# Kernel optimization log

Hardware: AMD Instinct MI355X
Metric: run time of the kernel (lower is better)

The kernel has to match this reference:

```python
import jax, jax.numpy as jnp
import numpy as np

IN_F, OUT_F, GRID = 1024, 1024, 8
B = 8192
GRID_LO, GRID_HI = -1.0, 1.0


def setup_inputs() -> dict:
    key = jax.random.key(0)
    k1, k2 = jax.random.split(key)
    x = jax.random.normal(k1, (B, IN_F), dtype=jnp.float32)
    # buffers: grid is linspace expanded over in_features; sigma = 1.5*h
    h = (GRID_HI - GRID_LO) / (GRID - 1)
    grid = jnp.broadcast_to(jnp.linspace(GRID_LO, GRID_HI, GRID, dtype=jnp.float32), (IN_F, GRID))
    sigma = jnp.float32(1.5 * h)
    # params
    scale_base = jnp.ones((IN_F, OUT_F), dtype=jnp.float32)
    scale_spline = jnp.ones((IN_F, OUT_F), dtype=jnp.float32)
    # kaiming_uniform-ish init: bound = sqrt(6/fan_in)/sqrt(1+a^2) approximated by small uniform
    fan_in = IN_F * GRID
    gain = np.sqrt(2.0 / (1.0 + 5.0 * 0.1 * 0.1))
    bound = gain * np.sqrt(3.0 / fan_in)
    spline_weight = jax.random.uniform(k2, (OUT_F, IN_F, GRID), dtype=jnp.float32, minval=-bound, maxval=bound)
    return {"x": x, "scale_base": scale_base, "spline_weight": spline_weight,
            "scale_spline": scale_spline, "grid": grid, "sigma": sigma}


def reference(x, scale_base, spline_weight, scale_spline, grid, sigma):
    # x: [B, I]; grid: [I, G]; spline_weight: [O, I, G]; scales: [I, O]
    base_out = jnp.einsum('bi,io->bo', jax.nn.silu(x), scale_base)
    # RBF bases: exp(-((x - grid)/sigma)^2)  -> [B, I, G]
    bases = jnp.exp(-jnp.square((x[:, :, None] - grid[None, :, :]) / sigma))
    # fused spline contraction (mathematically identical to big,oig->bio then bio,io->bo)
    spline_out = jnp.einsum('big,oig,io->bo', bases, spline_weight, scale_spline)
    return base_out + spline_out
```

## Files before the change

kernel.cpp:

```cpp
#include <hip/hip_runtime.h>


#define BATCH 8192
#define IN_F  1024
#define OUT_F 1024
#define GRID_N 8
#define K2    (IN_F * GRID_N)
#define KTOT  (IN_F + K2)

#define BM 128
#define BN 128
#define BK 64
#define BK8 128

typedef __bf16 bf16x8 __attribute__((ext_vector_type(8)));
typedef float  f32x4  __attribute__((ext_vector_type(4)));
typedef int    int32x8 __attribute__((ext_vector_type(8)));

__device__ __forceinline__ void gl2lds16(const void* g, void* l) {
  __builtin_amdgcn_global_load_lds(
      (const __attribute__((address_space(1))) void*)g,
      (__attribute__((address_space(3))) void*)l, 16, 0, 0);
}

__device__ __forceinline__ void pack_fp8x8(const float* v, int& w0, int& w1) {
  w0 = 0; w1 = 0;
  w0 = __builtin_amdgcn_cvt_pk_fp8_f32(v[0], v[1], w0, false);
  w0 = __builtin_amdgcn_cvt_pk_fp8_f32(v[2], v[3], w0, true);
  w1 = __builtin_amdgcn_cvt_pk_fp8_f32(v[4], v[5], w1, false);
  w1 = __builtin_amdgcn_cvt_pk_fp8_f32(v[6], v[7], w1, true);
}

__global__ __launch_bounds__(256)
void kan_mix(const float* __restrict__ x, const float* __restrict__ sb,
             const float* __restrict__ sw, const float* __restrict__ ss,
             const float* __restrict__ grid, const float* __restrict__ sigma,
             __bf16* __restrict__ sbT, unsigned char* __restrict__ wbt8,
             unsigned char* __restrict__ Ab8, __bf16* __restrict__ sbA) {
  const int t = threadIdx.x;
  const int bx = blockIdx.x;
  if (bx < 256) {
    __shared__ float tile[64][65];
    const int o0 = (bx & 15) * 64, k0 = (bx >> 4) * 64;
    const int r = t >> 4, c4 = (t & 15) * 4;
    #pragma unroll
    for (int it = 0; it < 4; ++it) {
      const int k = k0 + r + it * 16;
      float4 v = *(const float4*)(sb + (size_t)k * OUT_F + o0 + c4);
      tile[r + it * 16][c4 + 0] = v.x; tile[r + it * 16][c4 + 1] = v.y;
      tile[r + it * 16][c4 + 2] = v.z; tile[r + it * 16][c4 + 3] = v.w;
    }
    __syncthreads();
    #pragma unroll
    for (int it = 0; it < 4; ++it) {
      const int ol = r + it * 16;
      union { __bf16 h[4]; uint2 q; } s;
      #pragma unroll
      for (int e = 0; e < 4; ++e) s.h[e] = (__bf16)tile[c4 + e][ol];
      *(uint2*)(sbT + (size_t)(o0 + ol) * IN_F + k0 + c4) = s.q;
    }
  } else if (bx < 512) {
    __shared__ float tile[64][65];
    const int sp = bx - 256;
    const int o0 = (sp >> 4) * 64;
    const int j0 = (sp & 15) * 512;
    const int i0 = j0 >> 3;
    const int r = t >> 4, c4 = (t & 15) * 4;
    #pragma unroll
    for (int it = 0; it < 4; ++it) {
      const int i = i0 + r + it * 16;
      float4 v = *(const float4*)(ss + (size_t)i * OUT_F + o0 + c4);
      tile[r + it * 16][c4 + 0] = v.x; tile[r + it * 16][c4 + 1] = v.y;
      tile[r + it * 16][c4 + 2] = v.z; tile[r + it * 16][c4 + 3] = v.w;
    }
    __syncthreads();
    #pragma unroll
    for (int p = 0; p < 16; ++p) {
      const int f = p * 256 + t;
      const int o_l = f >> 6, i_l = f & 63;
      const float sc = tile[i_l][o_l];
      const float* swp = sw + (size_t)(o0 + o_l) * K2 + j0 + i_l * 8;
      float4 a = *(const float4*)swp;
      float4 b = *(const float4*)(swp + 4);
      float vv[8] = {a.x * sc, a.y * sc, a.z * sc, a.w * sc,
                     b.x * sc, b.y * sc, b.z * sc, b.w * sc};
      int w0, w1; pack_fp8x8(vv, w0, w1);
      *(int2*)(wbt8 + (size_t)(o0 + o_l) * K2 + j0 + i_l * 8) = make_int2(w0, w1);
    }
  } else {
    const int b = bx - 512;
    const float inv_sigma = 1.0f / sigma[0];
    const float* xrow = x + (size_t)b * IN_F;
    unsigned char* arow = Ab8 + (size_t)b * K2;
    __bf16* srow = sbA + (size_t)b * IN_F;
    {
      float4 v = ((const float4*)xrow)[t];
      float vv[4] = {v.x, v.y, v.z, v.w};
      union { __bf16 h[4]; uint2 q; } s;
      #pragma unroll
      for (int e = 0; e < 4; ++e) s.h[e] = (__bf16)(vv[e] / (1.0f + __expf(-vv[e])));
      ((uint2*)srow)[t] = s.q;
    }
    #pragma unroll
    for (int it = 0; it < 4; ++it) {
      const int i = t + it * 256;
      const float u = xrow[i];
      float4 g0 = *(const float4*)(grid + (size_t)i * GRID_N);
      float4 g1 = *(const float4*)(grid + (size_t)i * GRID_N + 4);
      float gg[8] = {g0.x, g0.y, g0.z, g0.w, g1.x, g1.y, g1.z, g1.w};
      float bb[8];
      #pragma unroll
      for (int g = 0; g < GRID_N; ++g) {
        float d = (u - gg[g]) * inv_sigma;
        bb[g] = __expf(-d * d);
      }
      int w0, w1; pack_fp8x8(bb, w0, w1);
      *(int2*)(arow + (size_t)i * GRID_N) = make_int2(w0, w1);
    }
  }
}

__global__ __launch_bounds__(256)
void kan_gemm_all(const unsigned char* __restrict__ Ab8,
                  const unsigned char* __restrict__ wbt8,
                  const __bf16* __restrict__ sbA,
                  const __bf16* __restrict__ sbT,
                  float* __restrict__ out) {
  __shared__ unsigned char As8[BM * BK8];
  __shared__ unsigned char Bs8[BN * BK8];
  __bf16* As16 = (__bf16*)As8;
  __bf16* Bs16 = (__bf16*)Bs8;

  const int tid = threadIdx.x;
  const int bx  = blockIdx.x;
  const int s   = bx >> 3;
  const int r0  = ((bx & 7) * 8 + (s >> 3)) * BM;
  const int c0  = (s & 7) * BN;

  const int lane = tid & 63, wave = tid >> 6;
  const int wm = wave & 1, wn = wave >> 1;
  const int quad = lane >> 4, l15 = lane & 15;

  int a_off8[4][2], b_off8[4][2];
  #pragma unroll
  for (int t4 = 0; t4 < 4; ++t4) {
    const int rowA = wm * 64 + t4 * 16 + l15;
    const int rowB = wn * 64 + t4 * 16 + l15;
    #pragma unroll
    for (int h = 0; h < 2; ++h) {
      a_off8[t4][h] = rowA * BK8 + (((quad * 2 + h) ^ (rowA & 7)) * 16);
      b_off8[t4][h] = rowB * BK8 + (((quad * 2 + h) ^ (rowB & 7)) * 16);
    }
  }
  int a_off16[2][4], b_off16[2][4];
  #pragma unroll
  for (int ks = 0; ks < 2; ++ks) {
    const int kc = ks * 4 + quad;
    #pragma unroll
    for (int t4 = 0; t4 < 4; ++t4) {
      const int rowA = wm * 64 + t4 * 16 + l15;
      a_off16[ks][t4] = (rowA * 8 + (kc ^ (rowA & 7))) * 8;
      const int rowB = wn * 64 + t4 * 16 + l15;
      b_off16[ks][t4] = (rowB * 8 + (kc ^ (rowB & 7))) * 8;
    }
  }
  const unsigned char* aSrc8[4]; const unsigned char* bSrc8[4];
  const __bf16* aSrc16[4]; const __bf16* bSrc16[4]; int dstOff[4];
  #pragma unroll
  for (int it = 0; it < 4; ++it) {
    const int p = it * 256 + tid;
    const int row = p >> 3;
    const int kc  = (p & 7) ^ (row & 7);
    aSrc8[it]  = Ab8  + (size_t)(r0 + row) * K2 + kc * 16;
    bSrc8[it]  = wbt8 + (size_t)(c0 + row) * K2 + kc * 16;
    aSrc16[it] = sbA  + (size_t)(r0 + row) * IN_F + kc * 8;
    bSrc16[it] = sbT  + (size_t)(c0 + row) * IN_F + kc * 8;
    dstOff[it] = p * 16;
  }

  f32x4 zero; zero[0] = 0.f; zero[1] = 0.f; zero[2] = 0.f; zero[3] = 0.f;
  f32x4 acc[4][4];
  #pragma unroll
  for (int a = 0; a < 4; ++a)
    #pragma unroll
    for (int b = 0; b < 4; ++b) acc[a][b] = zero;

  for (int kb = 0; kb < K2; kb += BK8) {
    __syncthreads();
    #pragma unroll
    for (int it = 0; it < 4; ++it) {
      gl2lds16(aSrc8[it] + kb, &As8[dstOff[it]]);
      gl2lds16(bSrc8[it] + kb, &Bs8[dstOff[it]]);
    }
    __syncthreads();
    union frag { int32x8 v; uint4 q[2]; };
    frag af[4], bfv[4];
    #pragma unroll
    for (int t4 = 0; t4 < 4; ++t4) {
      af[t4].q[0]  = *(const uint4*)&As8[a_off8[t4][0]];
      af[t4].q[1]  = *(const uint4*)&As8[a_off8[t4][1]];
      bfv[t4].q[0] = *(const uint4*)&Bs8[b_off8[t4][0]];
      bfv[t4].q[1] = *(const uint4*)&Bs8[b_off8[t4][1]];
    }
    #pragma unroll
    for (int tm = 0; tm < 4; ++tm)
      #pragma unroll
      for (int tn = 0; tn < 4; ++tn)
        acc[tm][tn] = __builtin_amdgcn_mfma_scale_f32_16x16x128_f8f6f4(
            af[tm].v, bfv[tn].v, acc[tm][tn],
            0, 0, 0, 0x7F7F7F7F, 0, 0x7F7F7F7F);
  }

  for (int kb = 0; kb < IN_F; kb += BK) {
    __syncthreads();
    #pragma unroll
    for (int it = 0; it < 4; ++it) {
      gl2lds16(aSrc16[it] + kb, (char*)As16 + dstOff[it]);
      gl2lds16(bSrc16[it] + kb, (char*)Bs16 + dstOff[it]);
    }
    __syncthreads();
    #pragma unroll
    for (int ks = 0; ks < 2; ++ks) {
      bf16x8 af[4], bfv[4];
      #pragma unroll
      for (int t4 = 0; t4 < 4; ++t4) af[t4]  = *(const bf16x8*)&As16[a_off16[ks][t4]];
      #pragma unroll
      for (int t4 = 0; t4 < 4; ++t4) bfv[t4] = *(const bf16x8*)&Bs16[b_off16[ks][t4]];
      #pragma unroll
      for (int tm = 0; tm < 4; ++tm)
        #pragma unroll
        for (int tn = 0; tn < 4; ++tn)
          acc[tm][tn] = __builtin_amdgcn_mfma_f32_16x16x32_bf16(
              af[tm], bfv[tn], acc[tm][tn], 0, 0, 0);
    }
  }

  #pragma unroll
  for (int tm = 0; tm < 4; ++tm) {
    const int row = r0 + wm * 64 + tm * 16 + quad * 4;
    #pragma unroll
    for (int tn = 0; tn < 4; ++tn) {
      const int col = c0 + wn * 64 + tn * 16 + l15;
      float* op = out + (size_t)row * OUT_F + col;
      #pragma unroll
      for (int r = 0; r < 4; ++r)
        op[(size_t)r * OUT_F] = acc[tm][tn][r];
    }
  }
}

__global__ __launch_bounds__(256)
void kan_prep_w_full(const float* __restrict__ sb, const float* __restrict__ sw,
                     const float* __restrict__ ss, __bf16* __restrict__ wbt) {
  const int t = threadIdx.x;
  if (blockIdx.x < 256) {
    __shared__ float tile[64][65];
    const int o0 = (blockIdx.x & 15) * 64, k0 = (blockIdx.x >> 4) * 64;
    const int r = t >> 4, c4 = (t & 15) * 4;
    #pragma unroll
    for (int it = 0; it < 4; ++it) {
      const int k = k0 + r + it * 16;
      float4 v = *(const float4*)(sb + (size_t)k * OUT_F + o0 + c4);
      tile[r + it * 16][c4 + 0] = v.x; tile[r + it * 16][c4 + 1] = v.y;
      tile[r + it * 16][c4 + 2] = v.z; tile[r + it * 16][c4 + 3] = v.w;
    }
    __syncthreads();
    #pragma unroll
    for (int it = 0; it < 4; ++it) {
      const int ol = r + it * 16;
      union { __bf16 h[4]; uint2 q; } s;
      #pragma unroll
      for (int e = 0; e < 4; ++e) s.h[e] = (__bf16)tile[c4 + e][ol];
      *(uint2*)(wbt + (size_t)(o0 + ol) * KTOT + k0 + c4) = s.q;
    }
  } else {
    const size_t e = ((size_t)(blockIdx.x - 256) * 256 + t) * 8;
    const int o = (int)(e >> 13);
    const int j = (int)(e & 8191);
    const int i = j >> 3;
    const float sc = ss[(size_t)i * OUT_F + o];
    float4 a = *(const float4*)(sw + e);
    float4 b = *(const float4*)(sw + e + 4);
    float vv[8] = {a.x, a.y, a.z, a.w, b.x, b.y, b.z, b.w};
    union { __bf16 h[8]; uint4 q; } s;
    #pragma unroll
    for (int g = 0; g < 8; ++g) s.h[g] = (__bf16)(vv[g] * sc);
    *(uint4*)(wbt + (size_t)o * KTOT + IN_F + j) = s.q;
  }
}

__global__ __launch_bounds__(256, 2)
void kan_gemm_fused(const float* __restrict__ x, const __bf16* __restrict__ wbt,
                    const float* __restrict__ grid, const float* __restrict__ sigma,
                    float* __restrict__ out) {
  __shared__ __bf16 As[BM * BK];
  __shared__ __bf16 Bs[BN * BK];
  __shared__ float  gLds[IN_F * GRID_N];
  const int tid = threadIdx.x;
  const int bx  = blockIdx.x;
  const int c0  = (bx & 7) * BN;
  const int r0  = (bx >> 3) * BM;
  for (int idx = tid; idx < IN_F * GRID_N / 4; idx += 256)
    ((float4*)gLds)[idx] = ((const float4*)grid)[idx];
  const float inv_sigma = 1.0f / sigma[0];
  const int lane = tid & 63, wave = tid >> 6;
  const int wm = wave & 1, wn = wave >> 1;
  const int quad = lane >> 4, l15 = lane & 15;
  f32x4 zero; zero[0] = 0.f; zero[1] = 0.f; zero[2] = 0.f; zero[3] = 0.f;
  f32x4 acc[4][4];
  #pragma unroll
  for (int a = 0; a < 4; ++a)
    #pragma unroll
    for (int b = 0; b < 4; ++b) acc[a][b] = zero;
  const int m = tid >> 1, half = tid & 1;
  const float* xrow = x + (size_t)(r0 + m) * IN_F;
  __syncthreads();
  for (int kb = 0; kb < KTOT; kb += BK) {
    union { __bf16 h[32]; uint4 q[4]; } av;
    if (kb < IN_F) {
      const float4* xp = (const float4*)(xrow + kb + half * 32);
      #pragma unroll
      for (int j4 = 0; j4 < 8; ++j4) {
        float4 v = xp[j4];
        float vv[4] = {v.x, v.y, v.z, v.w};
        #pragma unroll
        for (int e = 0; e < 4; ++e)
          av.h[j4 * 4 + e] = (__bf16)(vv[e] / (1.0f + __expf(-vv[e])));
      }
    } else {
      const int i0 = (kb - IN_F) >> 3;
      float4 xv = *(const float4*)(xrow + i0 + half * 4);
      float xs[4] = {xv.x, xv.y, xv.z, xv.w};
      #pragma unroll
      for (int ii = 0; ii < 4; ++ii) {
        const float u = xs[ii];
        const float* gp = &gLds[(i0 + half * 4 + ii) * GRID_N];
        #pragma unroll
        for (int g = 0; g < GRID_N; ++g) {
          float d = (u - gp[g]) * inv_sigma;
          av.h[ii * 8 + g] = (__bf16)__expf(-d * d);
        }
      }
    }
    __syncthreads();
    {
      uint4* dst = (uint4*)&As[m * BK + half * 32];
      #pragma unroll
      for (int qd = 0; qd < 4; ++qd) dst[qd] = av.q[qd];
    }
    #pragma unroll
    for (int it = 0; it < 4; ++it) {
      const int idx = it * 2048 + tid * 8;
      const int n = idx >> 6, k = idx & 63;
      gl2lds16(wbt + (size_t)(c0 + n) * KTOT + kb + k, &Bs[idx]);
    }
    __syncthreads();
    #pragma unroll
    for (int ks = 0; ks < 2; ++ks) {
      bf16x8 af[4], bfv[4];
      #pragma unroll
      for (int t4 = 0; t4 < 4; ++t4)
        af[t4] = *(const bf16x8*)&As[(wm * 64 + t4 * 16 + l15) * BK + ks * 32 + quad * 8];
      #pragma unroll
      for (int t4 = 0; t4 < 4; ++t4)
        bfv[t4] = *(const bf16x8*)&Bs[(wn * 64 + t4 * 16 + l15) * BK + ks * 32 + quad * 8];
      #pragma unroll
      for (int tm = 0; tm < 4; ++tm)
        #pragma unroll
        for (int tn = 0; tn < 4; ++tn)
          acc[tm][tn] = __builtin_amdgcn_mfma_f32_16x16x32_bf16(
              af[tm], bfv[tn], acc[tm][tn], 0, 0, 0);
    }
  }
  #pragma unroll
  for (int tm = 0; tm < 4; ++tm) {
    const int row = r0 + wm * 64 + tm * 16 + quad * 4;
    #pragma unroll
    for (int tn = 0; tn < 4; ++tn) {
      const int col = c0 + wn * 64 + tn * 16 + l15;
      float* op = out + (size_t)row * OUT_F + col;
      #pragma unroll
      for (int r = 0; r < 4; ++r)
        op[(size_t)r * OUT_F] = acc[tm][tn][r];
    }
  }
}

extern "C" void kernel_launch(void* const* d_in, const int* in_sizes, int n_in,
                              void* d_out, int out_size, void* d_ws, size_t ws_size,
                              hipStream_t stream) {
  const float* x     = (const float*)d_in[0];
  const float* sb    = (const float*)d_in[1];
  const float* sw    = (const float*)d_in[2];
  const float* ss    = (const float*)d_in[3];
  const float* grid  = (const float*)d_in[4];
  const float* sigma = (const float*)d_in[5];
  float* out = (float*)d_out;

  const size_t SBT_BYTES = (size_t)OUT_F * IN_F * 2;
  const size_t WS_BYTES  = (size_t)OUT_F * K2;
  const size_t A_BYTES   = (size_t)BATCH * K2;
  const size_t SBA_BYTES = (size_t)BATCH * IN_F * 2;

  if (ws_size >= SBT_BYTES + WS_BYTES + A_BYTES + SBA_BYTES) {
    __bf16*        sbT  = (__bf16*)d_ws;
    unsigned char* wbt8 = (unsigned char*)d_ws + SBT_BYTES;
    unsigned char* Ab8  = (unsigned char*)d_ws + SBT_BYTES + WS_BYTES;
    __bf16*        sbA  = (__bf16*)((char*)d_ws + SBT_BYTES + WS_BYTES + A_BYTES);
    kan_mix<<<dim3(512 + BATCH), dim3(256), 0, stream>>>(
        x, sb, sw, ss, grid, sigma, sbT, wbt8, Ab8, sbA);
    kan_gemm_all<<<dim3((BATCH / BM) * (OUT_F / BN)), dim3(256), 0, stream>>>(
        Ab8, wbt8, sbA, sbT, out);
  } else {
    __bf16* wbt = (__bf16*)d_ws;
    kan_prep_w_full<<<dim3(4352), dim3(256), 0, stream>>>(sb, sw, ss, wbt);
    kan_gemm_fused<<<dim3((BATCH / BM) * (OUT_F / BN)), dim3(256), 0, stream>>>(
        x, wbt, grid, sigma, out);
  }
}
```

Baseline: 221.2 us.

## Double-buffer LDS in fused KAN GEMM with 256x128 tiles and 8 waves

Restructures the combined fp8/bf16 GEMM to use two LDS buffers, so the global-to-LDS loads for the next K-slice are issued before the MFMAs on the current one, leaving one barrier per iteration instead of two. The block tile grows to 256x128 with 512 threads (4x2 waves), which halves the grid and shares each B tile across twice as many A rows. The fp8-to-bf16 phase change is handled by prefetching the first bf16 slice during the last fp8 iteration. MFMA sections are wrapped in s_setprio to favour issuing math. The cost is 96KB of LDS per block, which limits occupancy to one block per CU, and only 256 blocks in the grid.

Result: slower. 244.3 us (+10.4%).

```diff
diff --git a/kernel.cpp b/kernel.cpp
--- a/kernel.cpp
+++ b/kernel.cpp
@@ -120,25 +120,22 @@
   }
 }
 
-__global__ __launch_bounds__(256)
+__global__ __launch_bounds__(512, 2)
 void kan_gemm_all(const unsigned char* __restrict__ Ab8,
                   const unsigned char* __restrict__ wbt8,
                   const __bf16* __restrict__ sbA,
                   const __bf16* __restrict__ sbT,
                   float* __restrict__ out) {
-  __shared__ unsigned char As8[BM * BK8];
-  __shared__ unsigned char Bs8[BN * BK8];
-  __bf16* As16 = (__bf16*)As8;
-  __bf16* Bs16 = (__bf16*)Bs8;
+  __shared__ unsigned char smem[2][49152];
 
   const int tid = threadIdx.x;
   const int bx  = blockIdx.x;
-  const int s   = bx >> 3;
-  const int r0  = ((bx & 7) * 8 + (s >> 3)) * BM;
-  const int c0  = (s & 7) * BN;
+  const int xcd = bx & 7, loc = bx >> 3;
+  const int r0 = (xcd * 4 + (loc >> 3)) * 256;
+  const int c0 = (loc & 7) * 128;
 
   const int lane = tid & 63, wave = tid >> 6;
-  const int wm = wave & 1, wn = wave >> 1;
+  const int wm = wave & 3, wn = wave >> 2;
   const int quad = lane >> 4, l15 = lane & 15;
 
   int a_off8[4][2], b_off8[4][2];
@@ -148,8 +145,8 @@
     const int rowB = wn * 64 + t4 * 16 + l15;
     #pragma unroll
     for (int h = 0; h < 2; ++h) {
-      a_off8[t4][h] = rowA * BK8 + (((quad * 2 + h) ^ (rowA & 7)) * 16);
-      b_off8[t4][h] = rowB * BK8 + (((quad * 2 + h) ^ (rowB & 7)) * 16);
+      a_off8[t4][h] = rowA * 128 + (((quad * 2 + h) ^ (rowA & 7)) * 16);
+      b_off8[t4][h] = 32768 + rowB * 128 + (((quad * 2 + h) ^ (rowB & 7)) * 16);
     }
   }
   int a_off16[2][4], b_off16[2][4];
@@ -159,23 +156,31 @@
     #pragma unroll
     for (int t4 = 0; t4 < 4; ++t4) {
       const int rowA = wm * 64 + t4 * 16 + l15;
-      a_off16[ks][t4] = (rowA * 8 + (kc ^ (rowA & 7))) * 8;
+      a_off16[ks][t4] = (rowA * 8 + (kc ^ (rowA & 7))) * 16;
       const int rowB = wn * 64 + t4 * 16 + l15;
-      b_off16[ks][t4] = (rowB * 8 + (kc ^ (rowB & 7))) * 8;
-    }
-  }
-  const unsigned char* aSrc8[4]; const unsigned char* bSrc8[4];
-  const __bf16* aSrc16[4]; const __bf16* bSrc16[4]; int dstOff[4];
+      b_off16[ks][t4] = 32768 + (rowB * 8 + (kc ^ (rowB & 7))) * 16;
+    }
+  }
+
+  const unsigned char* aS8[4]; const __bf16* aS16[4]; int aD[4];
   #pragma unroll
   for (int it = 0; it < 4; ++it) {
-    const int p = it * 256 + tid;
+    const int p = it * 512 + tid;
     const int row = p >> 3;
     const int kc  = (p & 7) ^ (row & 7);
-    aSrc8[it]  = Ab8  + (size_t)(r0 + row) * K2 + kc * 16;
-    bSrc8[it]  = wbt8 + (size_t)(c0 + row) * K2 + kc * 16;
-    aSrc16[it] = sbA  + (size_t)(r0 + row) * IN_F + kc * 8;
-    bSrc16[it] = sbT  + (size_t)(c0 + row) * IN_F + kc * 8;
-    dstOff[it] = p * 16;
+    aS8[it]  = Ab8 + (size_t)(r0 + row) * K2 + kc * 16;
+    aS16[it] = sbA + (size_t)(r0 + row) * IN_F + kc * 8;
+    aD[it] = p * 16;
+  }
+  const unsigned char* bS8[2]; const __bf16* bS16[2]; int bD[2];
+  #pragma unroll
+  for (int it = 0; it < 2; ++it) {
+    const int q = it * 512 + tid;
+    const int row = q >> 3;
+    const int kc  = (q & 7) ^ (row & 7);
+    bS8[it]  = wbt8 + (size_t)(c0 + row) * K2 + kc * 16;
+    bS16[it] = sbT + (size_t)(c0 + row) * IN_F + kc * 8;
+    bD[it] = 32768 + q * 16;
   }
 
   f32x4 zero; zero[0] = 0.f; zero[1] = 0.f; zero[2] = 0.f; zero[3] = 0.f;
@@ -185,23 +190,38 @@
     #pragma unroll
     for (int b = 0; b < 4; ++b) acc[a][b] = zero;
 
-  for (int kb = 0; kb < K2; kb += BK8) {
-    __syncthreads();
-    #pragma unroll
-    for (int it = 0; it < 4; ++it) {
-      gl2lds16(aSrc8[it] + kb, &As8[dstOff[it]]);
-      gl2lds16(bSrc8[it] + kb, &Bs8[dstOff[it]]);
-    }
-    __syncthreads();
+  #pragma unroll
+  for (int it = 0; it < 4; ++it) gl2lds16(aS8[it], &smem[0][aD[it]]);
+  #pragma unroll
+  for (int it = 0; it < 2; ++it) gl2lds16(bS8[it], &smem[0][bD[it]]);
+  __syncthreads();
+
+  int cur = 0;
+  for (int t = 0; t < 64; ++t) {
+    const int nxt = cur ^ 1;
+    if (t < 63) {
+      const int kb = (t + 1) * BK8;
+      #pragma unroll
+      for (int it = 0; it < 4; ++it) gl2lds16(aS8[it] + kb, &smem[nxt][aD[it]]);
+      #pragma unroll
+      for (int it = 0; it < 2; ++it) gl2lds16(bS8[it] + kb, &smem[nxt][bD[it]]);
+    } else {
+      #pragma unroll
+      for (int it = 0; it < 4; ++it) gl2lds16(aS16[it], &smem[nxt][aD[it]]);
+      #pragma unroll
+      for (int it = 0; it < 2; ++it) gl2lds16(bS16[it], &smem[nxt][bD[it]]);
+    }
+    const unsigned char* sp = smem[cur];
     union frag { int32x8 v; uint4 q[2]; };
     frag af[4], bfv[4];
     #pragma unroll
     for (int t4 = 0; t4 < 4; ++t4) {
-      af[t4].q[0]  = *(const uint4*)&As8[a_off8[t4][0]];
-      af[t4].q[1]  = *(const uint4*)&As8[a_off8[t4][1]];
-      bfv[t4].q[0] = *(const uint4*)&Bs8[b_off8[t4][0]];
-      bfv[t4].q[1] = *(const uint4*)&Bs8[b_off8[t4][1]];
-    }
+      af[t4].q[0]  = *(const uint4*)(sp + a_off8[t4][0]);
+      af[t4].q[1]  = *(const uint4*)(sp + a_off8[t4][1]);
+      bfv[t4].q[0] = *(const uint4*)(sp + b_off8[t4][0]);
+      bfv[t4].q[1] = *(const uint4*)(sp + b_off8[t4][1]);
+    }
+    __builtin_amdgcn_s_setprio(1);
     #pragma unroll
     for (int tm = 0; tm < 4; ++tm)
       #pragma unroll
@@ -209,30 +229,39 @@
         acc[tm][tn] = __builtin_amdgcn_mfma_scale_f32_16x16x128_f8f6f4(
             af[tm].v, bfv[tn].v, acc[tm][tn],
             0, 0, 0, 0x7F7F7F7F, 0, 0x7F7F7F7F);
-  }
-
-  for (int kb = 0; kb < IN_F; kb += BK) {
-    __syncthreads();
-    #pragma unroll
-    for (int it = 0; it < 4; ++it) {
-      gl2lds16(aSrc16[it] + kb, (char*)As16 + dstOff[it]);
-      gl2lds16(bSrc16[it] + kb, (char*)Bs16 + dstOff[it]);
-    }
-    __syncthreads();
+    __builtin_amdgcn_s_setprio(0);
+    __syncthreads();
+    cur = nxt;
+  }
+
+  for (int t = 0; t < 16; ++t) {
+    const int nxt = cur ^ 1;
+    if (t < 15) {
+      const int ke = (t + 1) * BK;
+      #pragma unroll
+      for (int it = 0; it < 4; ++it) gl2lds16(aS16[it] + ke, &smem[nxt][aD[it]]);
+      #pragma unroll
+      for (int it = 0; it < 2; ++it) gl2lds16(bS16[it] + ke, &smem[nxt][bD[it]]);
+    }
+    const unsigned char* sp = smem[cur];
     #pragma unroll
     for (int ks = 0; ks < 2; ++ks) {
       bf16x8 af[4], bfv[4];
       #pragma unroll
-      for (int t4 = 0; t4 < 4; ++t4) af[t4]  = *(const bf16x8*)&As16[a_off16[ks][t4]];
-      #pragma unroll
-      for (int t4 = 0; t4 < 4; ++t4) bfv[t4] = *(const bf16x8*)&Bs16[b_off16[ks][t4]];
+      for (int t4 = 0; t4 < 4; ++t4) af[t4]  = *(const bf16x8*)(sp + a_off16[ks][t4]);
+      #pragma unroll
+      for (int t4 = 0; t4 < 4; ++t4) bfv[t4] = *(const bf16x8*)(sp + b_off16[ks][t4]);
+      __builtin_amdgcn_s_setprio(1);
       #pragma unroll
       for (int tm = 0; tm < 4; ++tm)
         #pragma unroll
         for (int tn = 0; tn < 4; ++tn)
           acc[tm][tn] = __builtin_amdgcn_mfma_f32_16x16x32_bf16(
               af[tm], bfv[tn], acc[tm][tn], 0, 0, 0);
-    }
+      __builtin_amdgcn_s_setprio(0);
+    }
+    __syncthreads();
+    cur = nxt;
   }
 
   #pragma unroll
@@ -409,7 +438,7 @@
     __bf16*        sbA  = (__bf16*)((char*)d_ws + SBT_BYTES + WS_BYTES + A_BYTES);
     kan_mix<<<dim3(512 + BATCH), dim3(256), 0, stream>>>(
         x, sb, sw, ss, grid, sigma, sbT, wbt8, Ab8, sbA);
-    kan_gemm_all<<<dim3((BATCH / BM) * (OUT_F / BN)), dim3(256), 0, stream>>>(
+    kan_gemm_all<<<dim3((BATCH / 256) * (OUT_F / 128)), dim3(512), 0, stream>>>(
         Ab8, wbt8, sbA, sbT, out);
   } else {
     __bf16* wbt = (__bf16*)d_ws;
```

## Double-buffer LDS tiles and prefetch next K-slice during MFMA compute

Applied to the files above, without the earlier changes.

Replaces the single-buffered load/sync/compute loops with a two-stage LDS ping-pong buffer. The global-to-LDS load of the next K tile is issued before the current tile is computed, and a partial vmcnt wait lets one stage of loads stay in flight. The transition from the fp8 phase to the bf16 phase is also prefetched, and MFMA sections are wrapped in s_setprio to favour compute. LDS use doubles to 64KB per block, which may reduce occupancy, and the manual waitcnt accounting is fragile.

Measured after the change: 224.8 us. Within noise of the previous version (+1.6%).

```diff
diff --git a/kernel.cpp b/kernel.cpp
--- a/kernel.cpp
+++ b/kernel.cpp
@@ -126,10 +126,7 @@
                   const __bf16* __restrict__ sbA,
                   const __bf16* __restrict__ sbT,
                   float* __restrict__ out) {
-  __shared__ unsigned char As8[BM * BK8];
-  __shared__ unsigned char Bs8[BN * BK8];
-  __bf16* As16 = (__bf16*)As8;
-  __bf16* Bs16 = (__bf16*)Bs8;
+  __shared__ unsigned char smem[2][32768];
 
   const int tid = threadIdx.x;
   const int bx  = blockIdx.x;
@@ -149,7 +146,7 @@
     #pragma unroll
     for (int h = 0; h < 2; ++h) {
       a_off8[t4][h] = rowA * BK8 + (((quad * 2 + h) ^ (rowA & 7)) * 16);
-      b_off8[t4][h] = rowB * BK8 + (((quad * 2 + h) ^ (rowB & 7)) * 16);
+      b_off8[t4][h] = 16384 + rowB * BK8 + (((quad * 2 + h) ^ (rowB & 7)) * 16);
     }
   }
   int a_off16[2][4], b_off16[2][4];
@@ -159,11 +156,12 @@
     #pragma unroll
     for (int t4 = 0; t4 < 4; ++t4) {
       const int rowA = wm * 64 + t4 * 16 + l15;
-      a_off16[ks][t4] = (rowA * 8 + (kc ^ (rowA & 7))) * 8;
+      a_off16[ks][t4] = (rowA * 8 + (kc ^ (rowA & 7))) * 16;
       const int rowB = wn * 64 + t4 * 16 + l15;
-      b_off16[ks][t4] = (rowB * 8 + (kc ^ (rowB & 7))) * 8;
-    }
-  }
+      b_off16[ks][t4] = 16384 + (rowB * 8 + (kc ^ (rowB & 7))) * 16;
+    }
+  }
+
   const unsigned char* aSrc8[4]; const unsigned char* bSrc8[4];
   const __bf16* aSrc16[4]; const __bf16* bSrc16[4]; int dstOff[4];
   #pragma unroll
@@ -185,23 +183,43 @@
     #pragma unroll
     for (int b = 0; b < 4; ++b) acc[a][b] = zero;
 
-  for (int kb = 0; kb < K2; kb += BK8) {
-    __syncthreads();
-    #pragma unroll
-    for (int it = 0; it < 4; ++it) {
-      gl2lds16(aSrc8[it] + kb, &As8[dstOff[it]]);
-      gl2lds16(bSrc8[it] + kb, &Bs8[dstOff[it]]);
-    }
-    __syncthreads();
+  #pragma unroll
+  for (int it = 0; it < 4; ++it) {
+    gl2lds16(aSrc8[it], &smem[0][dstOff[it]]);
+    gl2lds16(bSrc8[it], &smem[0][16384 + dstOff[it]]);
+  }
+
+  int cur = 0;
+  for (int t = 0; t < 64; ++t) {
+    const int nxt = cur ^ 1;
+    if (t < 63) {
+      const int kb = (t + 1) * BK8;
+      #pragma unroll
+      for (int it = 0; it < 4; ++it) {
+        gl2lds16(aSrc8[it] + kb, &smem[nxt][dstOff[it]]);
+        gl2lds16(bSrc8[it] + kb, &smem[nxt][16384 + dstOff[it]]);
+      }
+    } else {
+      #pragma unroll
+      for (int it = 0; it < 4; ++it) {
+        gl2lds16(aSrc16[it], &smem[nxt][dstOff[it]]);
+        gl2lds16(bSrc16[it], &smem[nxt][16384 + dstOff[it]]);
+      }
+    }
+    asm volatile("s_waitcnt vmcnt(8)" ::: "memory");
+    __builtin_amdgcn_s_barrier();
+    asm volatile("" ::: "memory");
+    const unsigned char* sp = smem[cur];
     union frag { int32x8 v; uint4 q[2]; };
     frag af[4], bfv[4];
     #pragma unroll
     for (int t4 = 0; t4 < 4; ++t4) {
-      af[t4].q[0]  = *(const uint4*)&As8[a_off8[t4][0]];
-      af[t4].q[1]  = *(const uint4*)&As8[a_off8[t4][1]];
-      bfv[t4].q[0] = *(const uint4*)&Bs8[b_off8[t4][0]];
-      bfv[t4].q[1] = *(const uint4*)&Bs8[b_off8[t4][1]];
-    }
+      af[t4].q[0]  = *(const uint4*)(sp + a_off8[t4][0]);
+      af[t4].q[1]  = *(const uint4*)(sp + a_off8[t4][1]);
+      bfv[t4].q[0] = *(const uint4*)(sp + b_off8[t4][0]);
+      bfv[t4].q[1] = *(const uint4*)(sp + b_off8[t4][1]);
+    }
+    __builtin_amdgcn_s_setprio(1);
     #pragma unroll
     for (int tm = 0; tm < 4; ++tm)
       #pragma unroll
@@ -209,30 +227,49 @@
         acc[tm][tn] = __builtin_amdgcn_mfma_scale_f32_16x16x128_f8f6f4(
             af[tm].v, bfv[tn].v, acc[tm][tn],
             0, 0, 0, 0x7F7F7F7F, 0, 0x7F7F7F7F);
-  }
-
-  for (int kb = 0; kb < IN_F; kb += BK) {
-    __syncthreads();
-    #pragma unroll
-    for (int it = 0; it < 4; ++it) {
-      gl2lds16(aSrc16[it] + kb, (char*)As16 + dstOff[it]);
-      gl2lds16(bSrc16[it] + kb, (char*)Bs16 + dstOff[it]);
-    }
-    __syncthreads();
+    __builtin_amdgcn_s_setprio(0);
+    asm volatile("" ::: "memory");
+    __builtin_amdgcn_s_barrier();
+    asm volatile("" ::: "memory");
+    cur = nxt;
+  }
+
+  for (int t = 0; t < 16; ++t) {
+    const int nxt = cur ^ 1;
+    if (t < 15) {
+      const int ke = (t + 1) * BK;
+      #pragma unroll
+      for (int it = 0; it < 4; ++it) {
+        gl2lds16(aSrc16[it] + ke, &smem[nxt][dstOff[it]]);
+        gl2lds16(bSrc16[it] + ke, &smem[nxt][16384 + dstOff[it]]);
+      }
+      asm volatile("s_waitcnt vmcnt(8)" ::: "memory");
+    } else {
+      asm volatile("s_waitcnt vmcnt(0)" ::: "memory");
+    }
+    __builtin_amdgcn_s_barrier();
+    asm volatile("" ::: "memory");
+    const unsigned char* sp = smem[cur];
     #pragma unroll
     for (int ks = 0; ks < 2; ++ks) {
       bf16x8 af[4], bfv[4];
       #pragma unroll
-      for (int t4 = 0; t4 < 4; ++t4) af[t4]  = *(const bf16x8*)&As16[a_off16[ks][t4]];
-      #pragma unroll
-      for (int t4 = 0; t4 < 4; ++t4) bfv[t4] = *(const bf16x8*)&Bs16[b_off16[ks][t4]];
+      for (int t4 = 0; t4 < 4; ++t4) af[t4]  = *(const bf16x8*)(sp + a_off16[ks][t4]);
+      #pragma unroll
+      for (int t4 = 0; t4 < 4; ++t4) bfv[t4] = *(const bf16x8*)(sp + b_off16[ks][t4]);
+      __builtin_amdgcn_s_setprio(1);
       #pragma unroll
       for (int tm = 0; tm < 4; ++tm)
         #pragma unroll
         for (int tn = 0; tn < 4; ++tn)
           acc[tm][tn] = __builtin_amdgcn_mfma_f32_16x16x32_bf16(
               af[tm], bfv[tn], acc[tm][tn], 0, 0, 0);
-    }
+      __builtin_amdgcn_s_setprio(0);
+    }
+    asm volatile("" ::: "memory");
+    __builtin_amdgcn_s_barrier();
+    asm volatile("" ::: "memory");
+    cur = nxt;
   }
 
   #pragma unroll
```
